# Optimization experiments

Measured on AMD Instinct MI355X. Metric: run time of the kernel, lower is better.

Reference implementation:

```python
import jax, jax.numpy as jnp
import numpy as np
from jax import lax

INPUT_DIM = 4
HIDDEN_DIM = 32
PRED_STEPS = 50
BATCH = 32768
SEQ_LEN = 200


def setup_inputs() -> dict:
    key = jax.random.key(0)
    ks = jax.random.split(key, 7)
    s = 1.0 / np.sqrt(HIDDEN_DIM)  # PyTorch LSTM init scale
    return {
        "history_data": jax.random.normal(ks[0], (BATCH, SEQ_LEN, INPUT_DIM), dtype=jnp.float32),
        "W_ih": jax.random.uniform(ks[1], (4 * HIDDEN_DIM, INPUT_DIM), jnp.float32, -s, s),
        "W_hh": jax.random.uniform(ks[2], (4 * HIDDEN_DIM, HIDDEN_DIM), jnp.float32, -s, s),
        "b_ih": jax.random.uniform(ks[3], (4 * HIDDEN_DIM,), jnp.float32, -s, s),
        "b_hh": jax.random.uniform(ks[4], (4 * HIDDEN_DIM,), jnp.float32, -s, s),
        "W_pred": jax.random.uniform(ks[5], (INPUT_DIM, HIDDEN_DIM), jnp.float32, -s, s),
        "b_pred": jax.random.uniform(ks[6], (INPUT_DIM,), jnp.float32, -s, s),
    }


def reference(history_data, W_ih, W_hh, b_ih, b_hh, W_pred, b_pred):
    H = W_hh.shape[1]
    b = b_ih + b_hh

    def cell(h, c, x):
        # PyTorch gate order: input, forget, cell(g), output
        gates = x @ W_ih.T + h @ W_hh.T + b  # [B, 4H]
        i, f, g, o = jnp.split(gates, 4, axis=-1)
        c_new = jax.nn.sigmoid(f) * c + jax.nn.sigmoid(i) * jnp.tanh(g)
        h_new = jax.nn.sigmoid(o) * jnp.tanh(c_new)
        return h_new, c_new

    B = history_data.shape[0]
    h0 = jnp.zeros((B, H), history_data.dtype)
    c0 = jnp.zeros((B, H), history_data.dtype)

    # Encode history: scan over time
    xs = jnp.swapaxes(history_data, 0, 1)  # [T, B, D]

    def hist_step(carry, x):
        h, c = carry
        h, c = cell(h, c, x)
        return (h, c), None

    (h, _), _ = lax.scan(hist_step, (h0, c0), xs)

    # each step (torch.zeros_like), carrying only h.
    def dec_step(h, _):
        pred = h @ W_pred.T + b_pred  # [B, INPUT_DIM]
        h_new, _ = cell(h, jnp.zeros_like(h), pred)
        return h_new, pred

    _, preds = lax.scan(dec_step, h, None, length=PRED_STEPS)  # [P, B, D]
    return jnp.swapaxes(preds, 0, 1)  # [B, PRED_STEPS, D]
```

## Files before the change

kernel.cpp:

```cpp
#include <hip/hip_runtime.h>
#include <math.h>

#define BATCH 32768
#define SEQLEN 200
#define PSTEPS 50
#define HID 32
#define LDS_PAD 36

typedef __attribute__((ext_vector_type(2))) _Float16 half2v;
typedef __attribute__((ext_vector_type(8))) _Float16 half8v;
typedef __attribute__((ext_vector_type(2))) __fp16   fp16x2;
typedef __attribute__((ext_vector_type(4))) float floatx4;

#define EXP2 __builtin_amdgcn_exp2f
#define RCPF __builtin_amdgcn_rcpf
#define PKRTZ __builtin_amdgcn_cvt_pkrtz

#define L1C 1.4426950408889634f
#define L2C 2.8853900817779268f

union H8 { unsigned int u[4]; half8v h; half2v h2[4]; };
union HU { fp16x2 h; unsigned int u; };

__device__ __forceinline__ unsigned int pk(float a, float b) {
    HU t; t.h = PKRTZ(a, b); return t.u;
}

__global__ __launch_bounds__(256, 2)
void lstm_mfma_kernel(const float* __restrict__ hist, const float* __restrict__ W_ih,
                      const float* __restrict__ W_hh, const float* __restrict__ b_ih,
                      const float* __restrict__ b_hh, const float* __restrict__ W_pred,
                      const float* __restrict__ b_pred, float* __restrict__ out)
{
    const int lane = threadIdx.x & 63;
    const int wv   = threadIdx.x >> 6;
    const int m    = lane & 15;
    const int quad = lane >> 4;
    const int elem0 = (blockIdx.x * 4 + wv) * 16;

    __shared__ __align__(16) float h_lds_all[4][16][LDS_PAD];
    float (*hl)[LDS_PAD] = h_lds_all[wv];

    half8v Bh[8], B2[8];
    #pragma unroll
    for (int n = 0; n < 8; ++n) {
        const int gc = n * 16 + m;
        H8 bh;
        #pragma unroll
        for (int jj = 0; jj < 4; ++jj) {
            bh.h2[jj] = (half2v){ (_Float16)W_hh[gc * HID + quad * 8 + 2 * jj],
                                  (_Float16)W_hh[gc * HID + quad * 8 + 2 * jj + 1] };
        }
        Bh[n] = bh.h;
        H8 b2; b2.u[0] = b2.u[1] = b2.u[2] = b2.u[3] = 0u;
        if (quad == 0) {
            b2.h2[0] = (half2v){ (_Float16)W_ih[gc * 4 + 0], (_Float16)W_ih[gc * 4 + 1] };
            b2.h2[1] = (half2v){ (_Float16)W_ih[gc * 4 + 2], (_Float16)W_ih[gc * 4 + 3] };
            float bsum = b_ih[gc] + b_hh[gc];
            _Float16 bhi = (_Float16)bsum;
            _Float16 blo = (_Float16)(bsum - (float)bhi);
            b2.h2[2] = (half2v){ bhi, blo };
        }
        B2[n] = b2.h;
    }
    const unsigned int one2 = 0x3C003C00u;

    float cst[2][4];
    #pragma unroll
    for (int hf = 0; hf < 2; ++hf)
        #pragma unroll
        for (int r = 0; r < 4; ++r) { cst[hf][r] = 0.f; hl[quad * 4 + r][hf * 16 + m] = 0.f; }
    asm volatile("s_waitcnt lgkmcnt(0)" ::: "memory");

    const float4* xp = (const float4*)(hist + (size_t)(elem0 + m) * (SEQLEN * 4));
    float4 xv = xp[0];
    #pragma unroll 1
    for (int t = 0; t < SEQLEN; ++t) {
        float4 h0 = *(const float4*)&hl[m][quad * 8];
        float4 h1 = *(const float4*)&hl[m][quad * 8 + 4];
        H8 ahu;
        ahu.u[0] = pk(h0.x, h0.y); ahu.u[1] = pk(h0.z, h0.w);
        ahu.u[2] = pk(h1.x, h1.y); ahu.u[3] = pk(h1.z, h1.w);
        const half8v ah = ahu.h;

        const unsigned int tx0 = pk(xv.x, xv.y), tx1 = pk(xv.z, xv.w);
        H8 a2u;
        a2u.u[0] = (quad == 0) ? tx0 : 0u;
        a2u.u[1] = (quad == 0) ? tx1 : 0u;
        a2u.u[2] = (quad == 0) ? one2 : 0u;
        a2u.u[3] = 0u;
        const half8v a2 = a2u.h;

        const int tn = (t + 1 < SEQLEN) ? t + 1 : SEQLEN - 1;
        float4 xn = xp[tn];

        floatx4 acc[8];
        #pragma unroll
        for (int n = 0; n < 8; ++n) {
            floatx4 a = __builtin_amdgcn_mfma_f32_16x16x32_f16(a2, B2[n], (floatx4){0.f,0.f,0.f,0.f}, 0, 0, 0);
            acc[n] = __builtin_amdgcn_mfma_f32_16x16x32_f16(ah, Bh[n], a, 0, 0, 0);
        }
        #pragma unroll
        for (int hf = 0; hf < 2; ++hf) {
            #pragma unroll
            for (int r = 0; r < 4; ++r) {
                const float gi = acc[0 + hf][r], gf = acc[2 + hf][r];
                const float gg = acc[4 + hf][r], go = acc[6 + hf][r];
                const float ei = EXP2(gi * -L1C);
                const float ef = EXP2(gf * -L1C);
                const float eo = EXP2(go * -L1C);
                const float eg = EXP2(gg * L2C);
                const float st = (eg - 1.0f) * RCPF((1.0f + ei) * (1.0f + eg));
                float cn = fmaf(RCPF(1.0f + ef), cst[hf][r], st);
                cn = fminf(fmaxf(cn, -30.0f), 30.0f);
                const float ec = EXP2(cn * L2C);
                const float hn = (ec - 1.0f) * RCPF((1.0f + eo) * (1.0f + ec));
                cst[hf][r] = cn;
                hl[quad * 4 + r][hf * 16 + m] = hn;
            }
        }
        asm volatile("s_waitcnt lgkmcnt(0)" ::: "memory");
        xv = xn;
    }

    float wp[4][8];
    #pragma unroll
    for (int d = 0; d < 4; ++d)
        #pragma unroll
        for (int j = 0; j < 8; ++j) wp[d][j] = W_pred[d * HID + quad * 8 + j];
    float bp[4] = { b_pred[0], b_pred[1], b_pred[2], b_pred[3] };

    float* op = out + (size_t)(elem0 + m) * (PSTEPS * 4);
    #pragma unroll 1
    for (int p = 0; p < PSTEPS; ++p) {
        float4 h0 = *(const float4*)&hl[m][quad * 8];
        float4 h1 = *(const float4*)&hl[m][quad * 8 + 4];
        const float hv[8] = { h0.x, h0.y, h0.z, h0.w, h1.x, h1.y, h1.z, h1.w };

        float pd[4];
        #pragma unroll
        for (int d = 0; d < 4; ++d) {
            float s = 0.f;
            #pragma unroll
            for (int j = 0; j < 8; ++j) s = fmaf(hv[j], wp[d][j], s);
            s += __shfl_xor(s, 16);
            s += __shfl_xor(s, 32);
            pd[d] = s + bp[d];
        }
        if (quad == 0) *(float4*)(op + p * 4) = make_float4(pd[0], pd[1], pd[2], pd[3]);

        if (p + 1 < PSTEPS) {
            H8 ahu;
            ahu.u[0] = pk(hv[0], hv[1]); ahu.u[1] = pk(hv[2], hv[3]);
            ahu.u[2] = pk(hv[4], hv[5]); ahu.u[3] = pk(hv[6], hv[7]);
            const half8v ah = ahu.h;
            const unsigned int tx0 = pk(pd[0], pd[1]), tx1 = pk(pd[2], pd[3]);
            H8 a2u;
            a2u.u[0] = (quad == 0) ? tx0 : 0u;
            a2u.u[1] = (quad == 0) ? tx1 : 0u;
            a2u.u[2] = (quad == 0) ? one2 : 0u;
            a2u.u[3] = 0u;
            const half8v a2 = a2u.h;

            floatx4 acc[6];
            #pragma unroll
            for (int nn = 0; nn < 6; ++nn) {
                const int n = (nn < 2) ? nn : nn + 2;
                floatx4 a = __builtin_amdgcn_mfma_f32_16x16x32_f16(a2, B2[n], (floatx4){0.f,0.f,0.f,0.f}, 0, 0, 0);
                acc[nn] = __builtin_amdgcn_mfma_f32_16x16x32_f16(ah, Bh[n], a, 0, 0, 0);
            }
            #pragma unroll
            for (int hf = 0; hf < 2; ++hf) {
                #pragma unroll
                for (int r = 0; r < 4; ++r) {
                    const float gi = acc[0 + hf][r], gg = acc[2 + hf][r], go = acc[4 + hf][r];
                    const float ei = EXP2(gi * -L1C);
                    const float eo = EXP2(go * -L1C);
                    const float eg = EXP2(gg * L2C);
                    const float cn = (eg - 1.0f) * RCPF((1.0f + ei) * (1.0f + eg));
                    const float ec = EXP2(cn * L2C);
                    const float hn = (ec - 1.0f) * RCPF((1.0f + eo) * (1.0f + ec));
                    hl[quad * 4 + r][hf * 16 + m] = hn;
                }
            }
            asm volatile("s_waitcnt lgkmcnt(0)" ::: "memory");
        }
    }
}

extern "C" void kernel_launch(void* const* d_in, const int* in_sizes, int n_in,
                              void* d_out, int out_size, void* d_ws, size_t ws_size,
                              hipStream_t stream) {
    const float* hist   = (const float*)d_in[0];
    const float* W_ih   = (const float*)d_in[1];
    const float* W_hh   = (const float*)d_in[2];
    const float* b_ih   = (const float*)d_in[3];
    const float* b_hh   = (const float*)d_in[4];
    const float* W_pred = (const float*)d_in[5];
    const float* b_pred = (const float*)d_in[6];
    float* out = (float*)d_out;

    const int blocks = (BATCH / 16) / 4;
    lstm_mfma_kernel<<<blocks, 256, 0, stream>>>(hist, W_ih, W_hh, b_ih, b_hh,
                                                 W_pred, b_pred, out);
}
```

Measured before the change: 429.3 us.

## Split each 16-sequence LSTM tile across two waves with double-buffered LDS

Each 16-element batch tile is now handled by two wavefronts, each computing half of the hidden units (4 gate MFMAs instead of 8 per wave). The hidden state is exchanged through a double-buffered LDS array with a workgroup barrier each step. The cell-state update is also refactored to use a single reciprocal. This halves the per-wave serial dependency chain per timestep and doubles the wave count, at the cost of a barrier per step and duplicated x loads and pointwise overheads.

```diff
diff --git a/kernel.cpp b/kernel.cpp
--- a/kernel.cpp
+++ b/kernel.cpp
@@ -26,32 +26,37 @@
     HU t; t.h = PKRTZ(a, b); return t.u;
 }
 
-__global__ __launch_bounds__(256, 2)
+__device__ __forceinline__ void lds_barrier() {
+    asm volatile("s_waitcnt lgkmcnt(0)" ::: "memory");
+    __builtin_amdgcn_s_barrier();
+    asm volatile("" ::: "memory");
+}
+
+__global__ __launch_bounds__(128, 4)
 void lstm_mfma_kernel(const float* __restrict__ hist, const float* __restrict__ W_ih,
                       const float* __restrict__ W_hh, const float* __restrict__ b_ih,
                       const float* __restrict__ b_hh, const float* __restrict__ W_pred,
                       const float* __restrict__ b_pred, float* __restrict__ out)
 {
     const int lane = threadIdx.x & 63;
-    const int wv   = threadIdx.x >> 6;
+    const int half = threadIdx.x >> 6;
     const int m    = lane & 15;
     const int quad = lane >> 4;
-    const int elem0 = (blockIdx.x * 4 + wv) * 16;
-
-    __shared__ __align__(16) float h_lds_all[4][16][LDS_PAD];
-    float (*hl)[LDS_PAD] = h_lds_all[wv];
-
-    half8v Bh[8], B2[8];
+    const int elem0 = blockIdx.x * 16;
+
+    __shared__ __align__(16) float hbuf[2][16][LDS_PAD];
+
+    half8v Bh[4], B2[4];
     #pragma unroll
-    for (int n = 0; n < 8; ++n) {
-        const int gc = n * 16 + m;
+    for (int g = 0; g < 4; ++g) {
+        const int gc = g * 32 + half * 16 + m;
         H8 bh;
         #pragma unroll
         for (int jj = 0; jj < 4; ++jj) {
             bh.h2[jj] = (half2v){ (_Float16)W_hh[gc * HID + quad * 8 + 2 * jj],
                                   (_Float16)W_hh[gc * HID + quad * 8 + 2 * jj + 1] };
         }
-        Bh[n] = bh.h;
+        Bh[g] = bh.h;
         H8 b2; b2.u[0] = b2.u[1] = b2.u[2] = b2.u[3] = 0u;
         if (quad == 0) {
             b2.h2[0] = (half2v){ (_Float16)W_ih[gc * 4 + 0], (_Float16)W_ih[gc * 4 + 1] };
@@ -61,23 +66,22 @@
             _Float16 blo = (_Float16)(bsum - (float)bhi);
             b2.h2[2] = (half2v){ bhi, blo };
         }
-        B2[n] = b2.h;
+        B2[g] = b2.h;
     }
     const unsigned int one2 = 0x3C003C00u;
 
-    float cst[2][4];
+    float cst[4];
     #pragma unroll
-    for (int hf = 0; hf < 2; ++hf)
-        #pragma unroll
-        for (int r = 0; r < 4; ++r) { cst[hf][r] = 0.f; hl[quad * 4 + r][hf * 16 + m] = 0.f; }
-    asm volatile("s_waitcnt lgkmcnt(0)" ::: "memory");
+    for (int r = 0; r < 4; ++r) { cst[r] = 0.f; hbuf[0][quad * 4 + r][half * 16 + m] = 0.f; }
+    lds_barrier();
 
     const float4* xp = (const float4*)(hist + (size_t)(elem0 + m) * (SEQLEN * 4));
     float4 xv = xp[0];
     #pragma unroll 1
     for (int t = 0; t < SEQLEN; ++t) {
-        float4 h0 = *(const float4*)&hl[m][quad * 8];
-        float4 h1 = *(const float4*)&hl[m][quad * 8 + 4];
+        const int rd = t & 1;
+        float4 h0 = *(const float4*)&hbuf[rd][m][quad * 8];
+        float4 h1 = *(const float4*)&hbuf[rd][m][quad * 8 + 4];
         H8 ahu;
         ahu.u[0] = pk(h0.x, h0.y); ahu.u[1] = pk(h0.z, h0.w);
         ahu.u[2] = pk(h1.x, h1.y); ahu.u[3] = pk(h1.z, h1.w);
@@ -94,32 +98,30 @@
         const int tn = (t + 1 < SEQLEN) ? t + 1 : SEQLEN - 1;
         float4 xn = xp[tn];
 
-        floatx4 acc[8];
-        #pragma unroll
-        for (int n = 0; n < 8; ++n) {
-            floatx4 a = __builtin_amdgcn_mfma_f32_16x16x32_f16(a2, B2[n], (floatx4){0.f,0.f,0.f,0.f}, 0, 0, 0);
-            acc[n] = __builtin_amdgcn_mfma_f32_16x16x32_f16(ah, Bh[n], a, 0, 0, 0);
-        }
-        #pragma unroll
-        for (int hf = 0; hf < 2; ++hf) {
-            #pragma unroll
-            for (int r = 0; r < 4; ++r) {
-                const float gi = acc[0 + hf][r], gf = acc[2 + hf][r];
-                const float gg = acc[4 + hf][r], go = acc[6 + hf][r];
-                const float ei = EXP2(gi * -L1C);
-                const float ef = EXP2(gf * -L1C);
-                const float eo = EXP2(go * -L1C);
-                const float eg = EXP2(gg * L2C);
-                const float st = (eg - 1.0f) * RCPF((1.0f + ei) * (1.0f + eg));
-                float cn = fmaf(RCPF(1.0f + ef), cst[hf][r], st);
-                cn = fminf(fmaxf(cn, -30.0f), 30.0f);
-                const float ec = EXP2(cn * L2C);
-                const float hn = (ec - 1.0f) * RCPF((1.0f + eo) * (1.0f + ec));
-                cst[hf][r] = cn;
-                hl[quad * 4 + r][hf * 16 + m] = hn;
-            }
-        }
-        asm volatile("s_waitcnt lgkmcnt(0)" ::: "memory");
+        floatx4 acc[4];
+        #pragma unroll
+        for (int g = 0; g < 4; ++g) {
+            floatx4 a = __builtin_amdgcn_mfma_f32_16x16x32_f16(a2, B2[g], (floatx4){0.f,0.f,0.f,0.f}, 0, 0, 0);
+            acc[g] = __builtin_amdgcn_mfma_f32_16x16x32_f16(ah, Bh[g], a, 0, 0, 0);
+        }
+        #pragma unroll
+        for (int r = 0; r < 4; ++r) {
+            const float gi = acc[0][r], gf = acc[1][r], gg = acc[2][r], go = acc[3][r];
+            const float ei = EXP2(gi * -L1C);
+            const float ef = EXP2(gf * -L1C);
+            const float eo = EXP2(go * -L1C);
+            const float eg = EXP2(gg * L2C);
+            const float pf = 1.0f + ef;
+            const float t1 = (1.0f + ei) * (1.0f + eg);
+            const float num = fmaf(cst[r], t1, (eg - 1.0f) * pf);
+            float cn = num * RCPF(t1 * pf);
+            cn = fminf(fmaxf(cn, -30.0f), 30.0f);
+            const float ec = EXP2(cn * L2C);
+            const float hn = (ec - 1.0f) * RCPF((1.0f + eo) * (1.0f + ec));
+            cst[r] = cn;
+            hbuf[rd ^ 1][quad * 4 + r][half * 16 + m] = hn;
+        }
+        lds_barrier();
         xv = xn;
     }
 
@@ -133,8 +135,9 @@
     float* op = out + (size_t)(elem0 + m) * (PSTEPS * 4);
     #pragma unroll 1
     for (int p = 0; p < PSTEPS; ++p) {
-        float4 h0 = *(const float4*)&hl[m][quad * 8];
-        float4 h1 = *(const float4*)&hl[m][quad * 8 + 4];
+        const int rd = p & 1;
+        float4 h0 = *(const float4*)&hbuf[rd][m][quad * 8];
+        float4 h1 = *(const float4*)&hbuf[rd][m][quad * 8 + 4];
         const float hv[8] = { h0.x, h0.y, h0.z, h0.w, h1.x, h1.y, h1.z, h1.w };
 
         float pd[4];
@@ -147,7 +150,7 @@
             s += __shfl_xor(s, 32);
             pd[d] = s + bp[d];
         }
-        if (quad == 0) *(float4*)(op + p * 4) = make_float4(pd[0], pd[1], pd[2], pd[3]);
+        if (half == 0 && quad == 0) *(float4*)(op + p * 4) = make_float4(pd[0], pd[1], pd[2], pd[3]);
 
         if (p + 1 < PSTEPS) {
             H8 ahu;
@@ -162,28 +165,25 @@
             a2u.u[3] = 0u;
             const half8v a2 = a2u.h;
 
-            floatx4 acc[6];
+            floatx4 acc[3];
             #pragma unroll
-            for (int nn = 0; nn < 6; ++nn) {
-                const int n = (nn < 2) ? nn : nn + 2;
-                floatx4 a = __builtin_amdgcn_mfma_f32_16x16x32_f16(a2, B2[n], (floatx4){0.f,0.f,0.f,0.f}, 0, 0, 0);
-                acc[nn] = __builtin_amdgcn_mfma_f32_16x16x32_f16(ah, Bh[n], a, 0, 0, 0);
+            for (int k = 0; k < 3; ++k) {
+                const int g = (k == 0) ? 0 : k + 1;
+                floatx4 a = __builtin_amdgcn_mfma_f32_16x16x32_f16(a2, B2[g], (floatx4){0.f,0.f,0.f,0.f}, 0, 0, 0);
+                acc[k] = __builtin_amdgcn_mfma_f32_16x16x32_f16(ah, Bh[g], a, 0, 0, 0);
             }
             #pragma unroll
-            for (int hf = 0; hf < 2; ++hf) {
-                #pragma unroll
-                for (int r = 0; r < 4; ++r) {
-                    const float gi = acc[0 + hf][r], gg = acc[2 + hf][r], go = acc[4 + hf][r];
-                    const float ei = EXP2(gi * -L1C);
-                    const float eo = EXP2(go * -L1C);
-                    const float eg = EXP2(gg * L2C);
-                    const float cn = (eg - 1.0f) * RCPF((1.0f + ei) * (1.0f + eg));
-                    const float ec = EXP2(cn * L2C);
-                    const float hn = (ec - 1.0f) * RCPF((1.0f + eo) * (1.0f + ec));
-                    hl[quad * 4 + r][hf * 16 + m] = hn;
-                }
+            for (int r = 0; r < 4; ++r) {
+                const float gi = acc[0][r], gg = acc[1][r], go = acc[2][r];
+                const float ei = EXP2(gi * -L1C);
+                const float eo = EXP2(go * -L1C);
+                const float eg = EXP2(gg * L2C);
+                const float cn = (eg - 1.0f) * RCPF((1.0f + ei) * (1.0f + eg));
+                const float ec = EXP2(cn * L2C);
+                const float hn = (ec - 1.0f) * RCPF((1.0f + eo) * (1.0f + ec));
+                hbuf[rd ^ 1][quad * 4 + r][half * 16 + m] = hn;
             }
-            asm volatile("s_waitcnt lgkmcnt(0)" ::: "memory");
+            lds_barrier();
         }
     }
 }
@@ -200,7 +200,7 @@
     const float* b_pred = (const float*)d_in[6];
     float* out = (float*)d_out;
 
-    const int blocks = (BATCH / 16) / 4;
-    lstm_mfma_kernel<<<blocks, 256, 0, stream>>>(hist, W_ih, W_hh, b_ih, b_hh,
+    const int blocks = BATCH / 16;
+    lstm_mfma_kernel<<<blocks, 128, 0, stream>>>(hist, W_ih, W_hh, b_ih, b_hh,
                                                  W_pred, b_pred, out);
 }
```

Measured after the change: 433.4 us. Within noise of the previous version (+1.0%).
